# Kernel tuning notes

Measured on AMD Instinct MI355X. Metric: run time of the kernel, lower is better.

Reference implementation:

```python
import jax, jax.numpy as jnp
import numpy as np

NUM_EMB = 8192
EMB_DIM = 32
LATENT = 1024
COMMIT = 0.25
CB_COST = 1.0


def _l2norm(x, eps=1e-12):
    # matches torch F.normalize: x / max(||x||, eps)
    n = jnp.sqrt(jnp.sum(x * x, axis=-1, keepdims=True))
    return x / jnp.maximum(n, eps)


def setup_inputs() -> dict:
    key = jax.random.key(0)
    k = jax.random.split(key, 6)
    B = 32768
    s_in = 1.0 / np.sqrt(LATENT)
    s_out = 1.0 / np.sqrt(EMB_DIM)
    return {
        "z_e": jax.random.normal(k[0], (B, LATENT), jnp.float32),
        "in_w": jax.random.uniform(k[1], (EMB_DIM, LATENT), jnp.float32, -s_in, s_in),
        "in_b": jax.random.uniform(k[2], (EMB_DIM,), jnp.float32, -s_in, s_in),
        "out_w": jax.random.uniform(k[3], (LATENT, EMB_DIM), jnp.float32, -s_out, s_out),
        "out_b": jax.random.uniform(k[4], (LATENT,), jnp.float32, -s_out, s_out),
        "codebook": jax.random.normal(k[5], (NUM_EMB, EMB_DIM), jnp.float32),
    }


def reference(z_e, in_w, in_b, out_w, out_b, codebook):
    # in_proj: [B, LATENT] -> [B, EMB_DIM]
    ze = z_e @ in_w.T + in_b
    zn = _l2norm(ze)                      # [B, E]
    wn = _l2norm(codebook)                # [Z, E]
    # squared euclidean distance between normalized vectors
    dist = (jnp.sum(zn * zn, axis=1, keepdims=True)
            - 2.0 * (zn @ wn.T)
            + jnp.sum(wn * wn, axis=1))   # [B, Z]
    idx = jnp.argmin(dist, axis=1)        # [B]
    z_q = codebook[idx]                   # [B, E] (unnormalized codebook lookup)
    enc_loss = jnp.mean((ze - jax.lax.stop_gradient(z_q)) ** 2)
    cb_loss = jnp.mean((z_q - jax.lax.stop_gradient(ze)) ** 2)
    loss = CB_COST * cb_loss + COMMIT * enc_loss
    # straight-through estimator
    z_st = ze + jax.lax.stop_gradient(z_q - ze)
    out = z_st @ out_w.T + out_b          # [B, LATENT]
    return out, loss, enc_loss, cb_loss, idx, ze
```

## Files before the change

### kernel.cpp

```cpp
#include <hip/hip_runtime.h>
#include <hip/hip_bf16.h>

#define B_SZ    32768
#define LAT     1024
#define EMB     32
#define ZCB     8192
#define NSPL    8
#define CPS     (ZCB / NSPL)
#define RESC_CAP 32768
#define EPS_MARGIN 2e-4f

#define OFF_LOSS  ((size_t)B_SZ * LAT)
#define OFF_ENC   (OFF_LOSS + 1)
#define OFF_CB    (OFF_LOSS + 2)
#define OFF_IDX   (OFF_LOSS + 3)
#define OFF_ZE    (OFF_IDX + B_SZ)

#define WS_PZE    0
#define WS_PB1    0
#define WS_PB2    262144
#define WS_PL15   524288
#define WS_ZEA    2097152
#define WS_ZNPK   3145728
#define WS_WPK    4194304
#define WS_IDXT   4456448
#define WS_CNT    4489216
#define WS_LIST   4489217
#define WS_LPART  4521985

typedef float  f32x4  __attribute__((ext_vector_type(4)));
typedef short  short8 __attribute__((ext_vector_type(8)));

__device__ __forceinline__ unsigned short f2bf(float x) {
    unsigned u = __float_as_uint(x);
    u += 0x7FFF + ((u >> 16) & 1);
    return (unsigned short)(u >> 16);
}
__device__ __forceinline__ float bf2f(unsigned short h) {
    return __uint_as_float(((unsigned)h) << 16);
}

__global__ __launch_bounds__(256) void knorm(const float* __restrict__ cb,
                                             short* __restrict__ wpk,
                                             int* __restrict__ cnt) {
    if (blockIdx.x == 0 && threadIdx.x == 0 && threadIdx.y == 0) *cnt = 0;
    int e = threadIdx.x;
    int r = threadIdx.y;
    int row = blockIdx.x * 8 + r;
    float v = cb[row * EMB + e];
    float s = v * v;
    #pragma unroll
    for (int m = 16; m >= 1; m >>= 1) s += __shfl_xor(s, m, 64);
    float n = fmaxf(sqrtf(s), 1e-12f);
    float w = v / n;
    unsigned short h = f2bf(w);
    unsigned short l = f2bf(w - bf2f(h));
    wpk[row * 64 + e]      = (short)h;
    wpk[row * 64 + 32 + e] = (short)l;
}

#define KZB 64
#define KZS 68
__global__ __launch_bounds__(256) void kze2(const float* __restrict__ z_e,
                                            const float* __restrict__ in_w,
                                            float* __restrict__ pze) {
    __shared__ float zs[64 * KZS];
    __shared__ float wt[KZB * 32];
    int tid = threadIdx.x;
    size_t row0 = (size_t)blockIdx.x * 64;
    int ks = blockIdx.y;
    int rs = tid >> 2;
    int eg = tid & 3;
    int E  = eg * 8;

    float acc[8];
    #pragma unroll
    for (int j = 0; j < 8; ++j) acc[j] = 0.f;

    for (int c = 0; c < 512 / KZB; ++c) {
        int kb = ks * 512 + c * KZB;
        __syncthreads();
        #pragma unroll
        for (int i = 0; i < 4; ++i) {
            int t = tid + i * 256;
            int r = t >> 4, c4 = t & 15;
            float4 v = *(const float4*)(z_e + (row0 + r) * LAT + kb + c4 * 4);
            *(float4*)&zs[r * KZS + c4 * 4] = v;
        }
        #pragma unroll
        for (int i = 0; i < 2; ++i) {
            int t = tid + i * 256;
            int e = t >> 4, k4 = t & 15;
            float4 v = *(const float4*)(in_w + (size_t)e * LAT + kb + k4 * 4);
            float vv[4] = {v.x, v.y, v.z, v.w};
            #pragma unroll
            for (int j = 0; j < 4; ++j) {
                int k = k4 * 4 + j;
                wt[k * 32 + (e ^ ((k & 7) << 2))] = vv[j];
            }
        }
        __syncthreads();
        #pragma unroll 4
        for (int kq = 0; kq < KZB / 4; ++kq) {
            int k0 = kq * 4;
            float4 za = *(const float4*)&zs[rs * KZS + k0];
            float zav[4] = {za.x, za.y, za.z, za.w};
            #pragma unroll
            for (int i = 0; i < 4; ++i) {
                int k = k0 + i;
                int sw = (k & 7) << 2;
                float4 w0 = *(const float4*)&wt[k * 32 + (E ^ sw)];
                float4 w1 = *(const float4*)&wt[k * 32 + ((E + 4) ^ sw)];
                float wa[8] = {w0.x, w0.y, w0.z, w0.w, w1.x, w1.y, w1.z, w1.w};
                #pragma unroll
                for (int j = 0; j < 8; ++j)
                    acc[j] = fmaf(zav[i], wa[j], acc[j]);
            }
        }
    }
    size_t rb = (size_t)ks * B_SZ + row0;
    float* p0 = pze + (rb + rs) * EMB + E;
    *(float4*)p0       = make_float4(acc[0], acc[1], acc[2], acc[3]);
    *(float4*)(p0 + 4) = make_float4(acc[4], acc[5], acc[6], acc[7]);
}

__global__ __launch_bounds__(256) void kprep(const float* __restrict__ pze,
                                             const float* __restrict__ in_b,
                                             float* __restrict__ ze_out,
                                             float* __restrict__ ze_a,
                                             short* __restrict__ znpk) {
    int tid = threadIdx.x;
    size_t row = (size_t)blockIdx.x * 64 + (tid >> 2);
    int eg = tid & 3;
    const float* p0 = pze + row * 32 + eg * 8;
    const float* p1 = p0 + (size_t)B_SZ * 32;
    float4 a0 = *(const float4*)p0, a1 = *(const float4*)(p0 + 4);
    float4 b0 = *(const float4*)p1, b1 = *(const float4*)(p1 + 4);
    float4 c0 = *(const float4*)(in_b + eg * 8), c1 = *(const float4*)(in_b + eg * 8 + 4);
    float v[8];
    v[0] = a0.x + b0.x + c0.x; v[1] = a0.y + b0.y + c0.y;
    v[2] = a0.z + b0.z + c0.z; v[3] = a0.w + b0.w + c0.w;
    v[4] = a1.x + b1.x + c1.x; v[5] = a1.y + b1.y + c1.y;
    v[6] = a1.z + b1.z + c1.z; v[7] = a1.w + b1.w + c1.w;
    float nn = 0.f;
    #pragma unroll
    for (int i = 0; i < 8; ++i) nn = fmaf(v[i], v[i], nn);
    nn += __shfl_xor(nn, 1, 64);
    nn += __shfl_xor(nn, 2, 64);
    float n = fmaxf(sqrtf(nn), 1e-12f);

    *(float4*)(ze_a + row * 32 + eg * 8)     = make_float4(v[0], v[1], v[2], v[3]);
    *(float4*)(ze_a + row * 32 + eg * 8 + 4) = make_float4(v[4], v[5], v[6], v[7]);
    #pragma unroll
    for (int i = 0; i < 8; ++i) ze_out[row * 32 + eg * 8 + i] = v[i];

    short8 hv, lv;
    #pragma unroll
    for (int i = 0; i < 8; ++i) {
        float x = v[i] / n;
        unsigned short h = f2bf(x);
        unsigned short l = f2bf(x - bf2f(h));
        hv[i] = (short)h; lv[i] = (short)l;
    }
    *(short8*)(znpk + row * 64 + eg * 8)      = hv;
    *(short8*)(znpk + row * 64 + 32 + eg * 8) = lv;
}

__global__ __launch_bounds__(256) void kdistM(const short* __restrict__ znpk,
                                              const short* __restrict__ wpk,
                                              float* __restrict__ pb1,
                                              float* __restrict__ pb2,
                                              int*   __restrict__ pl15) {
    __shared__ short wch[2][128 * 64];
    int tid = threadIdx.x;
    int wave = tid >> 6, l = tid & 63;
    int l15 = l & 15, g = l >> 4;
    size_t rowbase = (size_t)blockIdx.x * 256 + wave * 64;
    int s = blockIdx.y;

    short8 zh[4], zl[4];
    #pragma unroll
    for (int rt = 0; rt < 4; ++rt) {
        const short8* p = (const short8*)(znpk + (rowbase + rt * 16 + l15) * 64 + g * 8);
        zh[rt] = p[0];
        zl[rt] = p[4];
    }
    f32x4 zero4 = {0.f, 0.f, 0.f, 0.f};
    float bb1[16];
    #pragma unroll
    for (int i = 0; i < 16; ++i) bb1[i] = -1e30f;

    int sw = (l15 & 7) << 4;
    int bhoff = ((g * 16) ^ sw) >> 1;
    int bloff = ((64 + g * 16) ^ sw) >> 1;

    const short* wsrc = wpk + (size_t)s * CPS * 64;

#define STAGE_CHUNK(BUF, CC)                                                          \
    {                                                                                 \
        const char* wsb = (const char*)(wsrc + (size_t)(CC) * 128 * 64);              \
        _Pragma("unroll")                                                             \
        for (int i = 0; i < 4; ++i) {                                                 \
            int code0 = wave * 32 + i * 8 + (l >> 3);                                 \
            int sslot = (l & 7) ^ (code0 & 7);                                        \
            const void* gp = (const void*)(wsb + (size_t)code0 * 128 + sslot * 16);   \
            void* lp = (void*)&wch[BUF][(wave * 4096 + i * 1024) >> 1];               \
            __builtin_amdgcn_global_load_lds(                                         \
                (const __attribute__((address_space(1))) unsigned*)gp,                \
                (__attribute__((address_space(3))) unsigned*)lp, 16, 0, 0);           \
        }                                                                             \
    }

    STAGE_CHUNK(0, 0)
    __syncthreads();

    for (int c = 0; c < 8; ++c) {
        if (c + 1 < 8) STAGE_CHUNK((c + 1) & 1, c + 1)
        const short* W = &wch[c & 1][0];
        #pragma unroll
        for (int tt = 0; tt < 8; ++tt) {
            const short* rowp = W + (tt * 16 + l15) * 64;
            short8 bh = *(const short8*)(rowp + bhoff);
            short8 bl = *(const short8*)(rowp + bloff);
            #pragma unroll
            for (int rt = 0; rt < 4; ++rt) {
                f32x4 acc = __builtin_amdgcn_mfma_f32_16x16x32_bf16(zh[rt], bh, zero4, 0, 0, 0);
                acc = __builtin_amdgcn_mfma_f32_16x16x32_bf16(zl[rt], bh, acc, 0, 0, 0);
                acc = __builtin_amdgcn_mfma_f32_16x16x32_bf16(zh[rt], bl, acc, 0, 0, 0);
                #pragma unroll
                for (int r = 0; r < 4; ++r) {
                    int slot = rt * 4 + r;
                    bb1[slot] = fmaxf(bb1[slot], acc[r]);
                }
            }
        }
        __syncthreads();
    }
#undef STAGE_CHUNK
    #pragma unroll
    for (int slot = 0; slot < 16; ++slot) {
        float B1 = bb1[slot], B2 = -1e30f;
        int ID = l15;
        #pragma unroll
        for (int m = 1; m <= 8; m <<= 1) {
            float ob1 = __shfl_xor(B1, m, 64);
            float ob2 = __shfl_xor(B2, m, 64);
            int   oid = __shfl_xor(ID, m, 64);
            float mn = fminf(B1, ob1);
            B2 = fmaxf(fmaxf(B2, ob2), mn);
            bool take = (ob1 > B1) || (ob1 == B1 && oid < ID);
            B1 = take ? ob1 : B1;
            ID = take ? oid : ID;
        }
        if (l15 == 0) {
            size_t row = rowbase + (size_t)(slot >> 2) * 16 + g * 4 + (slot & 3);
            pb1[(size_t)s * B_SZ + row] = B1;
            pb2[(size_t)s * B_SZ + row] = B2;
            pl15[(size_t)s * B_SZ + row] = ID;
        }
    }
}

__global__ __launch_bounds__(256) void krecover(const float* __restrict__ ze_a,
                                                const float* __restrict__ cb,
                                                const float* __restrict__ pb1,
                                                const float* __restrict__ pb2,
                                                const int* __restrict__ pl15,
                                                int* __restrict__ idxt,
                                                int* __restrict__ cnt,
                                                int* __restrict__ list) {
    int tid = threadIdx.x;
    int l = tid & 63;
    int gl = l & 7;
    int gj = l >> 3;
    int row = blockIdx.x * 4 + (tid >> 6);

    float best1 = pb1[row], othv = pb2[row];
    int c = pl15[row], wsn = 0;
    #pragma unroll
    for (int s2 = 1; s2 < NSPL; ++s2) {
        float b  = pb1[(size_t)s2 * B_SZ + row];
        float sb = pb2[(size_t)s2 * B_SZ + row];
        int   li = pl15[(size_t)s2 * B_SZ + row];
        float mn = fminf(best1, b);
        othv = fmaxf(fmaxf(othv, sb), mn);
        if (b > best1) { best1 = b; c = li; wsn = s2; }
    }
    int s = wsn, lc = c;

    float4 z = *(const float4*)(ze_a + (size_t)row * 32 + gl * 4);
    float zz = fmaf(z.x, z.x, fmaf(z.y, z.y, fmaf(z.z, z.z, z.w * z.w)));
    zz += __shfl_xor(zz, 1, 64);
    zz += __shfl_xor(zz, 2, 64);
    zz += __shfl_xor(zz, 4, 64);
    float zinv = 1.f / fmaxf(sqrtf(zz), 1e-12f);
    z.x *= zinv; z.y *= zinv; z.z *= zinv; z.w *= zinv;

    float best = -1e30f; int bi = 0;
    #pragma unroll
    for (int b = 0; b < CPS / 16 / 8; ++b) {
        int t = b * 8 + gj;
        int j = s * CPS + t * 16 + lc;
        float4 w = *(const float4*)(cb + (size_t)j * 32 + gl * 4);
        float w2 = fmaf(w.x, w.x, fmaf(w.y, w.y, fmaf(w.z, w.z, w.w * w.w)));
        float dt = fmaf(z.x, w.x, fmaf(z.y, w.y, fmaf(z.z, w.z, z.w * w.w)));
        w2 += __shfl_xor(w2, 1, 64); dt += __shfl_xor(dt, 1, 64);
        w2 += __shfl_xor(w2, 2, 64); dt += __shfl_xor(dt, 2, 64);
        w2 += __shfl_xor(w2, 4, 64); dt += __shfl_xor(dt, 4, 64);
        float inv = 1.f / fmaxf(sqrtf(w2), 1e-12f);
        float m = dt * inv - 0.5f * (w2 * inv * inv);
        if (m > best || (m == best && j < bi)) { best = m; bi = j; }
    }
    #pragma unroll
    for (int mk = 8; mk <= 32; mk <<= 1) {
        float ob = __shfl_xor(best, mk, 64);
        int   oi = __shfl_xor(bi, mk, 64);
        bool take = (ob > best) || (ob == best && oi < bi);
        best = take ? ob : best;
        bi   = take ? oi : bi;
    }
    if (l == 0) {
        idxt[row] = bi;
        if (best - (othv - 0.5f) < EPS_MARGIN) {
            int p = atomicAdd(cnt, 1);
            if (p < RESC_CAP) list[p] = row;
        }
    }
}

__global__ __launch_bounds__(256) void krescore(const float* __restrict__ ze_a,
                                                const float* __restrict__ cb,
                                                int* __restrict__ idxt,
                                                const int* __restrict__ cnt,
                                                const int* __restrict__ list) {
    __shared__ float bvs[4];
    __shared__ int   bis[4];
    int tid = threadIdx.x;
    int wave = tid >> 6, l = tid & 63;
    int gl = l & 7;
    int gj = l >> 3;
    int n = *cnt; if (n > RESC_CAP) n = RESC_CAP;
    for (int ii = blockIdx.x; ii < n; ii += gridDim.x) {
        int row = list[ii];
        float4 z = *(const float4*)(ze_a + (size_t)row * 32 + gl * 4);
        float zz = fmaf(z.x, z.x, fmaf(z.y, z.y, fmaf(z.z, z.z, z.w * z.w)));
        zz += __shfl_xor(zz, 1, 64);
        zz += __shfl_xor(zz, 2, 64);
        zz += __shfl_xor(zz, 4, 64);
        float zinv = 1.f / fmaxf(sqrtf(zz), 1e-12f);
        z.x *= zinv; z.y *= zinv; z.z *= zinv; z.w *= zinv;

        float best = -1e30f; int bi = 0;
        int jbase = wave * 2048 + gj;
        for (int b = 0; b < 32; ++b) {
            float w2v[8], dtv[8];
            #pragma unroll
            for (int cc = 0; cc < 8; ++cc) {
                int j = jbase + (b * 8 + cc) * 8;
                float4 w = *(const float4*)(cb + (size_t)j * 32 + gl * 4);
                w2v[cc] = fmaf(w.x, w.x, fmaf(w.y, w.y, fmaf(w.z, w.z, w.w * w.w)));
                dtv[cc] = fmaf(z.x, w.x, fmaf(z.y, w.y, fmaf(z.z, w.z, z.w * w.w)));
            }
            #pragma unroll
            for (int cc = 0; cc < 8; ++cc) {
                w2v[cc] += __shfl_xor(w2v[cc], 1, 64);
                dtv[cc] += __shfl_xor(dtv[cc], 1, 64);
            }
            #pragma unroll
            for (int cc = 0; cc < 8; ++cc) {
                w2v[cc] += __shfl_xor(w2v[cc], 2, 64);
                dtv[cc] += __shfl_xor(dtv[cc], 2, 64);
            }
            #pragma unroll
            for (int cc = 0; cc < 8; ++cc) {
                w2v[cc] += __shfl_xor(w2v[cc], 4, 64);
                dtv[cc] += __shfl_xor(dtv[cc], 4, 64);
            }
            #pragma unroll
            for (int cc = 0; cc < 8; ++cc) {
                int j = jbase + (b * 8 + cc) * 8;
                float inv = 1.f / fmaxf(sqrtf(w2v[cc]), 1e-12f);
                float m = dtv[cc] * inv - 0.5f * (w2v[cc] * inv * inv);
                if (m > best || (m == best && j < bi)) { best = m; bi = j; }
            }
        }
        #pragma unroll
        for (int mk = 8; mk <= 32; mk <<= 1) {
            float ob = __shfl_xor(best, mk, 64);
            int   oi = __shfl_xor(bi, mk, 64);
            bool take = (ob > best) || (ob == best && oi < bi);
            best = take ? ob : best;
            bi   = take ? oi : bi;
        }
        if (l == 0) { bvs[wave] = best; bis[wave] = bi; }
        __syncthreads();
        if (tid == 0) {
            float B = bvs[0]; int I = bis[0];
            #pragma unroll
            for (int w2i = 1; w2i < 4; ++w2i) {
                float ob = bvs[w2i]; int oi = bis[w2i];
                if (ob > B || (ob == B && oi < I)) { B = ob; I = oi; }
            }
            idxt[row] = I;
        }
        __syncthreads();
    }
}

__global__ __launch_bounds__(256) void kout(const float* __restrict__ ze_a,
                                            const int* __restrict__ idxt,
                                            const float* __restrict__ cb,
                                            const float* __restrict__ out_w,
                                            const float* __restrict__ out_b,
                                            float* __restrict__ out,
                                            float* __restrict__ out_idx,
                                            float* __restrict__ lpart) {
    __shared__ float zsh[128 * EMB];
    __shared__ int ish[128];
    __shared__ float red[4];
    int tid = threadIdx.x;
    int col = blockIdx.x * 512 + tid * 2;
    size_t row0 = (size_t)blockIdx.y * 128;
    bool bx0 = (blockIdx.x == 0);
    if (tid < 128) ish[tid] = idxt[row0 + tid];
    __syncthreads();
    float sq = 0.f;
    #pragma unroll
    for (int i = 0; i < 4; ++i) {
        int flat = i * 256 + tid;
        int r = flat >> 3, q = flat & 7;
        float4 zv = *(const float4*)(ze_a + (row0 + r) * EMB + q * 4);
        float4 qv = *(const float4*)(cb + (size_t)ish[r] * EMB + q * 4);
        if (bx0) {
            float dx = zv.x - qv.x, dy = zv.y - qv.y, dz = zv.z - qv.z, dw = zv.w - qv.w;
            sq += (dx * dx + dy * dy) + (dz * dz + dw * dw);
        }
        float4 o;
        o.x = zv.x + (qv.x - zv.x); o.y = zv.y + (qv.y - zv.y);
        o.z = zv.z + (qv.z - zv.z); o.w = zv.w + (qv.w - zv.w);
        *(float4*)&zsh[r * EMB + q * 4] = o;
    }
    if (bx0) {
        #pragma unroll
        for (int m = 1; m <= 32; m <<= 1) sq += __shfl_xor(sq, m, 64);
        if ((tid & 63) == 0) red[tid >> 6] = sq;
    }
    float wa[32], wb[32];
    {
        const float4* wa4 = (const float4*)(out_w + (size_t)col * EMB);
        const float4* wb4 = (const float4*)(out_w + (size_t)(col + 1) * EMB);
        #pragma unroll
        for (int i = 0; i < 8; ++i) {
            float4 a = wa4[i]; wa[4*i]=a.x; wa[4*i+1]=a.y; wa[4*i+2]=a.z; wa[4*i+3]=a.w;
            float4 b = wb4[i]; wb[4*i]=b.x; wb[4*i+1]=b.y; wb[4*i+2]=b.z; wb[4*i+3]=b.w;
        }
    }
    float b0 = out_b[col], b1 = out_b[col + 1];
    __syncthreads();
    if (bx0) {
        if (tid == 0) lpart[blockIdx.y] = (red[0] + red[1]) + (red[2] + red[3]);
        if (tid < 128) out_idx[row0 + tid] = (float)ish[tid];
    }
    for (int rr = 0; rr < 128; ++rr) {
        const float4* zr4 = (const float4*)(zsh + rr * EMB);
        float a0 = b0, a1 = b1;
        #pragma unroll
        for (int q = 0; q < 8; ++q) {
            float4 z = zr4[q];
            a0 = fmaf(z.x, wa[4*q],   a0); a1 = fmaf(z.x, wb[4*q],   a1);
            a0 = fmaf(z.y, wa[4*q+1], a0); a1 = fmaf(z.y, wb[4*q+1], a1);
            a0 = fmaf(z.z, wa[4*q+2], a0); a1 = fmaf(z.z, wb[4*q+2], a1);
            a0 = fmaf(z.w, wa[4*q+3], a0); a1 = fmaf(z.w, wb[4*q+3], a1);
        }
        float2 o; o.x = a0; o.y = a1;
        *(float2*)(out + (row0 + rr) * LAT + col) = o;
    }
}

__global__ void kloss(const float* __restrict__ lpart, float* __restrict__ dout) {
    float v = lpart[threadIdx.x];
    #pragma unroll
    for (int m = 1; m <= 32; m <<= 1) v += __shfl_xor(v, m, 64);
    __shared__ float tmp[4];
    if ((threadIdx.x & 63) == 0) tmp[threadIdx.x >> 6] = v;
    __syncthreads();
    if (threadIdx.x == 0) {
        float enc = ((tmp[0] + tmp[1]) + (tmp[2] + tmp[3])) / (float)(B_SZ * EMB);
        dout[OFF_LOSS] = 1.0f * enc + 0.25f * enc;
        dout[OFF_ENC]  = enc;
        dout[OFF_CB]   = enc;
    }
}

extern "C" void kernel_launch(void* const* d_in, const int* in_sizes, int n_in,
                              void* d_out, int out_size, void* d_ws, size_t ws_size,
                              hipStream_t stream) {
    const float* z_e   = (const float*)d_in[0];
    const float* in_w  = (const float*)d_in[1];
    const float* in_b  = (const float*)d_in[2];
    const float* out_w = (const float*)d_in[3];
    const float* out_b = (const float*)d_in[4];
    const float* cb    = (const float*)d_in[5];

    float* out = (float*)d_out;
    float* ws  = (float*)d_ws;
    float* pze   = ws + WS_PZE;
    float* pb1   = ws + WS_PB1;
    float* pb2   = ws + WS_PB2;
    int*   pl15  = (int*)(ws + WS_PL15);
    float* ze_a  = ws + WS_ZEA;
    short* znpk  = (short*)(ws + WS_ZNPK);
    short* wpk   = (short*)(ws + WS_WPK);
    int*   idxt  = (int*)(ws + WS_IDXT);
    int*   cnt   = (int*)(ws + WS_CNT);
    int*   list  = (int*)(ws + WS_LIST);
    float* lpart = ws + WS_LPART;

    knorm   <<<dim3(ZCB / 8), dim3(32, 8), 0, stream>>>(cb, wpk, cnt);
    kze2    <<<dim3(B_SZ / 64, 2), 256, 0, stream>>>(z_e, in_w, pze);
    kprep   <<<dim3(B_SZ / 64), 256, 0, stream>>>(pze, in_b, out + OFF_ZE, ze_a, znpk);
    kdistM  <<<dim3(B_SZ / 256, NSPL), 256, 0, stream>>>(znpk, wpk, pb1, pb2, pl15);
    krecover<<<dim3(B_SZ / 4), 256, 0, stream>>>(ze_a, cb, pb1, pb2, pl15, idxt, cnt, list);
    krescore<<<dim3(512), 256, 0, stream>>>(ze_a, cb, idxt, cnt, list);
    kout    <<<dim3(2, B_SZ / 128), 256, 0, stream>>>(ze_a, idxt, cb, out_w, out_b, out,
                                                      out + OFF_IDX, lpart);
    kloss   <<<1, 256, 0, stream>>>(lpart, out);
}
```

Before: 250.1 us.

## Double-buffer in-proj z tiles with direct global-to-LDS async loads

Restructures the in-projection partial GEMM (kze2) to double-buffer the z_e tile in shared memory. The next tile is loaded with `__builtin_amdgcn_global_load_lds` (16-byte direct-to-LDS loads), and the next in_w chunk is prefetched into registers while the current tile is being computed. Row padding is replaced by an XOR swizzle of 16-byte chunks, so the direct-to-LDS layout stays conflict-light. The aim is to overlap the large z_e stream with FMA work and skip the register round-trip for z tiles, at the cost of twice the LDS for z and an extra barrier per iteration.

```diff
diff --git a/kernel.cpp b/kernel.cpp
--- a/kernel.cpp
+++ b/kernel.cpp
@@ -60,51 +60,70 @@
 }
 
 #define KZB 64
-#define KZS 68
 __global__ __launch_bounds__(256) void kze2(const float* __restrict__ z_e,
                                             const float* __restrict__ in_w,
                                             float* __restrict__ pze) {
-    __shared__ float zs[64 * KZS];
+    __shared__ float zs[2][64 * 64];
     __shared__ float wt[KZB * 32];
     int tid = threadIdx.x;
+    int wave = tid >> 6, l = tid & 63;
     size_t row0 = (size_t)blockIdx.x * 64;
     int ks = blockIdx.y;
     int rs = tid >> 2;
     int eg = tid & 3;
     int E  = eg * 8;
 
+    int e0 = tid >> 4,          k40 = tid & 15;
+    int e1 = (tid + 256) >> 4,  k41 = tid & 15;
+
+#define STAGE_Z(BUF, KB)                                                              \
+    {                                                                                 \
+        _Pragma("unroll")                                                             \
+        for (int i = 0; i < 4; ++i) {                                                 \
+            int r = i * 16 + wave * 4 + (l >> 4);                                     \
+            int sc = (l & 15) ^ (r & 7);                                              \
+            const void* gp = (const void*)(z_e + (row0 + r) * LAT + (KB) + sc * 4);   \
+            void* lp = (void*)&zs[BUF][i * 1024 + wave * 256];                        \
+            __builtin_amdgcn_global_load_lds(                                         \
+                (const __attribute__((address_space(1))) unsigned*)gp,                \
+                (__attribute__((address_space(3))) unsigned*)lp, 16, 0, 0);           \
+        }                                                                             \
+    }
+
     float acc[8];
     #pragma unroll
     for (int j = 0; j < 8; ++j) acc[j] = 0.f;
 
-    for (int c = 0; c < 512 / KZB; ++c) {
-        int kb = ks * 512 + c * KZB;
-        __syncthreads();
-        #pragma unroll
-        for (int i = 0; i < 4; ++i) {
-            int t = tid + i * 256;
-            int r = t >> 4, c4 = t & 15;
-            float4 v = *(const float4*)(z_e + (row0 + r) * LAT + kb + c4 * 4);
-            *(float4*)&zs[r * KZS + c4 * 4] = v;
-        }
-        #pragma unroll
-        for (int i = 0; i < 2; ++i) {
-            int t = tid + i * 256;
-            int e = t >> 4, k4 = t & 15;
-            float4 v = *(const float4*)(in_w + (size_t)e * LAT + kb + k4 * 4);
-            float vv[4] = {v.x, v.y, v.z, v.w};
-            #pragma unroll
-            for (int j = 0; j < 4; ++j) {
-                int k = k4 * 4 + j;
-                wt[k * 32 + (e ^ ((k & 7) << 2))] = vv[j];
-            }
-        }
-        __syncthreads();
+    {
+        int kb0 = ks * 512;
+        STAGE_Z(0, kb0)
+        float4 w0 = *(const float4*)(in_w + (size_t)e0 * LAT + kb0 + k40 * 4);
+        float4 w1 = *(const float4*)(in_w + (size_t)e1 * LAT + kb0 + k41 * 4);
+        float v0[4] = {w0.x, w0.y, w0.z, w0.w};
+        float v1[4] = {w1.x, w1.y, w1.z, w1.w};
+        #pragma unroll
+        for (int j = 0; j < 4; ++j) {
+            int k = k40 * 4 + j;
+            wt[k * 32 + (e0 ^ ((k & 7) << 2))] = v0[j];
+            wt[k * 32 + (e1 ^ ((k & 7) << 2))] = v1[j];
+        }
+    }
+    __syncthreads();
+
+    for (int c = 0; c < 8; ++c) {
+        float4 wp0, wp1;
+        if (c + 1 < 8) {
+            int kbn = ks * 512 + (c + 1) * KZB;
+            STAGE_Z((c + 1) & 1, kbn)
+            wp0 = *(const float4*)(in_w + (size_t)e0 * LAT + kbn + k40 * 4);
+            wp1 = *(const float4*)(in_w + (size_t)e1 * LAT + kbn + k41 * 4);
+        }
+        const float* Z = &zs[c & 1][0];
         #pragma unroll 4
         for (int kq = 0; kq < KZB / 4; ++kq) {
+            float4 za = *(const float4*)&Z[rs * 64 + ((kq ^ (rs & 7)) << 2)];
+            float zav[4] = {za.x, za.y, za.z, za.w};
             int k0 = kq * 4;
-            float4 za = *(const float4*)&zs[rs * KZS + k0];
-            float zav[4] = {za.x, za.y, za.z, za.w};
             #pragma unroll
             for (int i = 0; i < 4; ++i) {
                 int k = k0 + i;
@@ -117,7 +136,21 @@
                     acc[j] = fmaf(zav[i], wa[j], acc[j]);
             }
         }
-    }
+        __syncthreads();
+        if (c + 1 < 8) {
+            float v0[4] = {wp0.x, wp0.y, wp0.z, wp0.w};
+            float v1[4] = {wp1.x, wp1.y, wp1.z, wp1.w};
+            #pragma unroll
+            for (int j = 0; j < 4; ++j) {
+                int k = k40 * 4 + j;
+                wt[k * 32 + (e0 ^ ((k & 7) << 2))] = v0[j];
+                wt[k * 32 + (e1 ^ ((k & 7) << 2))] = v1[j];
+            }
+        }
+        __syncthreads();
+    }
+#undef STAGE_Z
+
     size_t rb = (size_t)ks * B_SZ + row0;
     float* p0 = pze + (rb + rs) * EMB + E;
     *(float4*)p0       = make_float4(acc[0], acc[1], acc[2], acc[3]);
```

After: 250.4 us. No clear change (+0.1%).
